# Performance work log

Hardware: AMD Instinct MI355X
Metric: run time of the kernel (lower is better)

## Reference

```python
import jax, jax.numpy as jnp
import numpy as np

NUM_EMBEDDINGS = 1024
EMBEDDING_DIM = 256


def setup_inputs() -> dict:
    key = jax.random.key(0)
    kx, kc = jax.random.split(key)
    x = jax.random.normal(kx, (32, 256, 64, 64), dtype=jnp.float32)
    # codebook initialized uniform(-1/K, 1/K) as in the torch module
    codebook = jax.random.uniform(
        kc, (NUM_EMBEDDINGS, EMBEDDING_DIM), dtype=jnp.float32,
        minval=-1.0 / NUM_EMBEDDINGS, maxval=1.0 / NUM_EMBEDDINGS)
    return {"x": x, "codebook": codebook}


def reference(x, codebook):
    # x: (B, C, H, W) -> (B, H, W, C) -> (N, C)
    B, C, H, W = x.shape
    xf = jnp.transpose(x, (0, 2, 3, 1)).reshape(-1, C)  # (N, C)
    dist = (jnp.sum(xf * xf, axis=1, keepdims=True)
            + jnp.sum(codebook * codebook, axis=1)
            - 2.0 * jnp.matmul(xf, codebook.T))
    indices = jnp.argmin(dist, axis=1)[:, None]  # (N, 1), matches torch unsqueeze(1)
    quantized = codebook[indices[:, 0]].reshape(B, H, W, C)  # gather
    quantized = jnp.transpose(quantized, (0, 3, 1, 2))  # (B, C, H, W)
    return indices, quantized
```

## Files before the change

kernel.cpp:

```cpp
#include <hip/hip_runtime.h>
#include <stdint.h>

#define CDIM   256
#define KCODES 1024
#define HWSZ   4096
#define NROWS  131072
#define DELTA_P 4.7e-4f

#define WS_BQ    0
#define WS_IDX   4096
#define WS_CBBF  528384
#define WS_CNT   1052672
#define WS_LIST  1052800
#define WS_SLOT  1577216

typedef __attribute__((ext_vector_type(8))) short short8;
typedef __attribute__((ext_vector_type(4))) float f32x4;

__device__ inline unsigned short bf16rne(float f) {
    uint32_t u = __float_as_uint(f);
    u += 0x7FFF + ((u >> 16) & 1);
    return (unsigned short)(u >> 16);
}

__device__ __forceinline__ unsigned umin32(unsigned a, unsigned b) { return a < b ? a : b; }
__device__ __forceinline__ unsigned umax32(unsigned a, unsigned b) { return a > b ? a : b; }

__device__ __forceinline__ unsigned long long packkey(float s, int k) {
    unsigned b = __float_as_uint(s);
    unsigned m = (b & 0x80000000u) ? ~b : (b | 0x80000000u);
    return ((unsigned long long)m << 32) | (unsigned)k;
}

__global__ void codesq_kernel(const float* __restrict__ cb, float* __restrict__ Bq) {
#pragma clang fp contract(off)
    int k = blockIdx.x * 256 + threadIdx.x;
    if (k >= KCODES) return;
    const float* er = cb + (size_t)k * CDIM;
    float half_s[2];
    for (int h = 0; h < 2; ++h) {
        float r[8];
        #pragma unroll
        for (int j = 0; j < 8; ++j) { float v = er[h*128 + j]; r[j] = v * v; }
        for (int i = 8; i < 128; i += 8) {
            #pragma unroll
            for (int j = 0; j < 8; ++j) { float v = er[h*128 + i + j]; float sq = v*v; r[j] = r[j] + sq; }
        }
        half_s[h] = ((r[0]+r[1]) + (r[2]+r[3])) + ((r[4]+r[5]) + (r[6]+r[7]));
    }
    Bq[k] = half_s[0] + half_s[1];
}

__global__ void cbcvt_kernel(const float* __restrict__ cb, unsigned short* __restrict__ cbbf,
                             int* __restrict__ counter) {
    int i = blockIdx.x * 256 + threadIdx.x;
    float4 v = ((const float4*)cb)[i];
    ushort4 o;
    o.x = bf16rne(v.x); o.y = bf16rne(v.y); o.z = bf16rne(v.z); o.w = bf16rne(v.w);
    ((ushort4*)cbbf)[i] = o;
    if (i == 0) *counter = 0;
}

__global__ __launch_bounds__(256, 2)
void screen_kernel(const float* __restrict__ x, const unsigned short* __restrict__ cbbf,
                   const float* __restrict__ Bq,
                   int* __restrict__ idx_out, float* __restrict__ outF,
                   int* __restrict__ flag_list, int* __restrict__ counter,
                   unsigned long long* __restrict__ slots) {
    __shared__ unsigned short xs[64 * 264];
    __shared__ unsigned int sRed[4][64][2];

    const int t = threadIdx.x;
    const int w = t >> 6, l = t & 63;
    const int l15 = l & 15, quad = l >> 4;
    const int r0 = blockIdx.x * 64;
    const float* xbase = x + (size_t)(r0 >> 12) * (CDIM * HWSZ) + (r0 & 4095);

    {
        int cbase = (t >> 4) * 2;
        int row4  = (t & 15) * 4;
        for (int it = 0; it < 8; ++it) {
            int c = cbase + it * 32;
            float4 fa = *(const float4*)(xbase + (size_t)c * HWSZ + row4);
            float4 fb = *(const float4*)(xbase + (size_t)(c + 1) * HWSZ + row4);
            *(uint32_t*)&xs[(row4+0)*264 + c] = (uint32_t)bf16rne(fa.x) | ((uint32_t)bf16rne(fb.x) << 16);
            *(uint32_t*)&xs[(row4+1)*264 + c] = (uint32_t)bf16rne(fa.y) | ((uint32_t)bf16rne(fb.y) << 16);
            *(uint32_t*)&xs[(row4+2)*264 + c] = (uint32_t)bf16rne(fa.z) | ((uint32_t)bf16rne(fb.z) << 16);
            *(uint32_t*)&xs[(row4+3)*264 + c] = (uint32_t)bf16rne(fa.w) | ((uint32_t)bf16rne(fb.w) << 16);
        }
    }

    __syncthreads();

    short8 af[8][4];
    #pragma unroll
    for (int step = 0; step < 8; ++step)
        #pragma unroll
        for (int rf = 0; rf < 4; ++rf)
            af[step][rf] = *(const short8*)&xs[(rf*16 + l15)*264 + step*32 + quad*8];

    const unsigned short* bbase = cbbf + (size_t)(w*32 + l15) * CDIM + quad * 8;
    const int kbase = w*32 + l15;

    unsigned int K1[16], K2[16];
    #pragma unroll
    for (int i = 0; i < 16; ++i) { K1[i] = 0xFFFFFFFFu; K2[i] = 0xFFFFFFFFu; }

    for (int kt = 0; kt < 8; ++kt) {
        float bqp0 = Bq[kt*128 + kbase]      + 0.75f;
        float bqp1 = Bq[kt*128 + kbase + 16] + 0.75f;

        f32x4 acc[4][2];
        #pragma unroll
        for (int rf = 0; rf < 4; ++rf)
            #pragma unroll
            for (int cf = 0; cf < 2; ++cf) acc[rf][cf] = (f32x4){0.f, 0.f, 0.f, 0.f};

        #pragma unroll
        for (int step = 0; step < 8; ++step) {
            int koff = step * 32;
            short8 bfr0 = *(const short8*)(bbase + (size_t)(kt*128)      * CDIM + koff);
            short8 bfr1 = *(const short8*)(bbase + (size_t)(kt*128 + 16) * CDIM + koff);
            #pragma unroll
            for (int rf = 0; rf < 4; ++rf) {
                acc[rf][0] = __builtin_amdgcn_mfma_f32_16x16x32_bf16(af[step][rf], bfr0, acc[rf][0], 0, 0, 0);
                acc[rf][1] = __builtin_amdgcn_mfma_f32_16x16x32_bf16(af[step][rf], bfr1, acc[rf][1], 0, 0, 0);
            }
        }

        unsigned int kk0 = (unsigned)(kt*128 + kbase);
        unsigned int kk1 = kk0 + 16u;
        #pragma unroll
        for (int rf = 0; rf < 4; ++rf)
            #pragma unroll
            for (int reg = 0; reg < 4; ++reg) {
                int st = rf*4 + reg;
                {
                    float s = fmaf(-2.f, acc[rf][0][reg], bqp0);
                    unsigned int key = (__float_as_uint(s) & 0xFFFFFC00u) | kk0;
                    unsigned int t1 = umin32(key, K1[st]);
                    unsigned int t2 = umax32(key, K1[st]);
                    K1[st] = t1;
                    K2[st] = umin32(t2, K2[st]);
                }
                {
                    float s = fmaf(-2.f, acc[rf][1][reg], bqp1);
                    unsigned int key = (__float_as_uint(s) & 0xFFFFFC00u) | kk1;
                    unsigned int t1 = umin32(key, K1[st]);
                    unsigned int t2 = umax32(key, K1[st]);
                    K1[st] = t1;
                    K2[st] = umin32(t2, K2[st]);
                }
            }
    }

    #pragma unroll
    for (int st = 0; st < 16; ++st) {
        #pragma unroll
        for (int m = 1; m < 16; m <<= 1) {
            unsigned int o1 = (unsigned int)__shfl_xor((int)K1[st], m, 64);
            unsigned int o2 = (unsigned int)__shfl_xor((int)K2[st], m, 64);
            unsigned int n2 = umin32(umax32(K1[st], o1), umin32(K2[st], o2));
            K1[st] = umin32(K1[st], o1);
            K2[st] = n2;
        }
    }
    if (l15 == 0) {
        #pragma unroll
        for (int rf = 0; rf < 4; ++rf)
            #pragma unroll
            for (int reg = 0; reg < 4; ++reg) {
                int r = rf*16 + quad*4 + reg;
                int st = rf*4 + reg;
                sRed[w][r][0] = K1[st];
                sRed[w][r][1] = K2[st];
            }
    }
    __syncthreads();
    if (t < 64) {
        unsigned int A1 = sRed[0][t][0], A2 = sRed[0][t][1];
        #pragma unroll
        for (int ww = 1; ww < 4; ++ww) {
            unsigned int B1 = sRed[ww][t][0], B2 = sRed[ww][t][1];
            unsigned int n2 = umin32(umax32(A1, B1), umin32(A2, B2));
            A1 = umin32(A1, B1);
            A2 = n2;
        }
        int row = r0 + t;
        int k1i = (int)(A1 & 1023u);
        idx_out[row] = k1i;
        outF[row] = (float)k1i;
        float v1 = __uint_as_float(A1 & 0xFFFFFC00u);
        float v2 = __uint_as_float(A2 & 0xFFFFFC00u);
        if (!(v2 - v1 > DELTA_P)) {
            int pos = atomicAdd(counter, 1);
            flag_list[pos] = row;
            slots[pos] = 0xFFFFFFFFFFFFFFFFull;
        }
    }
}

__global__ __launch_bounds__(256)
void rescore_kernel(const float* __restrict__ x, const float* __restrict__ cb,
                    const float* __restrict__ Bq,
                    const int* __restrict__ flag_list, const int* __restrict__ counter,
                    unsigned long long* __restrict__ slots) {
    __shared__ float xsh[64 * 256];
    __shared__ float cbs[64 * 256];
    __shared__ float sA[64];
    __shared__ int   rows_s[64];

    int cnt = *counter;
    int nbat = (cnt + 63) >> 6;
    int nwork = nbat * 4;
    for (int wk = blockIdx.x; wk < nwork; wk += gridDim.x) {
        int bat = wk >> 2;
        int wq  = wk & 3;
        __syncthreads();
        if (threadIdx.x < 64) {
            int j = bat * 64 + threadIdx.x;
            rows_s[threadIdx.x] = (j < cnt) ? flag_list[j] : -1;
        }
        __syncthreads();
        {
            int rr = threadIdx.x >> 2;
            int c0 = (threadIdx.x & 3) * 64;
            int row = rows_s[rr]; if (row < 0) row = rows_s[0];
            const float* xr = x + (size_t)(row >> 12) * (CDIM * HWSZ) + (row & 4095);
            #pragma unroll 8
            for (int j = 0; j < 64; ++j)
                xsh[rr*256 + c0 + j] = xr[(size_t)(c0 + j) * HWSZ];
        }
        __syncthreads();
        if (threadIdx.x < 64) {
#pragma clang fp contract(off)
            const float* xr = &xsh[threadIdx.x * 256];
            float hs[2];
            for (int h = 0; h < 2; ++h) {
                float rr8[8];
                #pragma unroll
                for (int j = 0; j < 8; ++j) { float v = xr[h*128 + j]; rr8[j] = v * v; }
                for (int i = 8; i < 128; i += 8) {
                    #pragma unroll
                    for (int j = 0; j < 8; ++j) { float v = xr[h*128 + i + j]; float sq = v*v; rr8[j] = rr8[j] + sq; }
                }
                hs[h] = ((rr8[0]+rr8[1]) + (rr8[2]+rr8[3])) + ((rr8[4]+rr8[5]) + (rr8[6]+rr8[7]));
            }
            sA[threadIdx.x] = hs[0] + hs[1];
        }
        __syncthreads();

        const int rq = threadIdx.x >> 4;
        const int cq = threadIdx.x & 15;
        const int sw = cq & 7;
        float Ar[4];
        #pragma unroll
        for (int i = 0; i < 4; ++i) Ar[i] = sA[rq*4 + i];

        float bv[4]; int bk[4];
        #pragma unroll
        for (int i = 0; i < 4; ++i) { bv[i] = 3.4e38f; bk[i] = 0; }

        for (int tile = 0; tile < 4; ++tile) {
            int kt0 = wq * 256 + tile * 64;
            __syncthreads();
            {
                int kc = threadIdx.x >> 2, seg = threadIdx.x & 3;
                const float* crow = cb + (size_t)(kt0 + kc) * CDIM + seg * 64;
                float* dst = &cbs[kc * 256];
                int kw = kc & 7;
                #pragma unroll
                for (int i = 0; i < 16; ++i) {
                    int lc = seg*16 + i;
                    *(float4*)&dst[(lc ^ kw) * 4] = *(const float4*)&crow[i*4];
                }
            }
            __syncthreads();
            float bq[4];
            #pragma unroll
            for (int j = 0; j < 4; ++j) bq[j] = Bq[kt0 + cq + j*16];

            const float* eb[4];
            #pragma unroll
            for (int j = 0; j < 4; ++j) eb[j] = &cbs[(cq + j*16) * 256];
            const float* xb[4];
            #pragma unroll
            for (int i = 0; i < 4; ++i) xb[i] = &xsh[(rq*4 + i) * 256];

            float acc[4][4];
            #pragma unroll
            for (int i = 0; i < 4; ++i)
                #pragma unroll
                for (int j = 0; j < 4; ++j) acc[i][j] = 0.f;

            #pragma unroll 2
            for (int c4 = 0; c4 < 64; ++c4) {
                int so = (c4 ^ sw) * 4;
                float4 ev[4], xv[4];
                #pragma unroll
                for (int j = 0; j < 4; ++j) ev[j] = *(const float4*)&eb[j][so];
                #pragma unroll
                for (int i = 0; i < 4; ++i) xv[i] = *(const float4*)&xb[i][c4*4];
                #pragma unroll
                for (int i = 0; i < 4; ++i)
                    #pragma unroll
                    for (int j = 0; j < 4; ++j) {
                        float a = acc[i][j];
                        a = fmaf(xv[i].x, ev[j].x, a);
                        a = fmaf(xv[i].y, ev[j].y, a);
                        a = fmaf(xv[i].z, ev[j].z, a);
                        a = fmaf(xv[i].w, ev[j].w, a);
                        acc[i][j] = a;
                    }
            }
            #pragma unroll
            for (int j = 0; j < 4; ++j) {
                int k = kt0 + cq + j*16;
                #pragma unroll
                for (int i = 0; i < 4; ++i) {
                    float T1 = Ar[i] + bq[j];
                    float s  = T1 - 2.0f * acc[i][j];
                    if (s < bv[i]) { bv[i] = s; bk[i] = k; }
                }
            }
        }
        #pragma unroll
        for (int i = 0; i < 4; ++i) {
            float b = bv[i]; int k = bk[i];
            #pragma unroll
            for (int m = 1; m < 16; m <<= 1) {
                float ov = __shfl_xor(b, m, 64);
                int   ok = __shfl_xor(k, m, 64);
                if (ov < b || (ov == b && ok < k)) { b = ov; k = ok; }
            }
            bv[i] = b; bk[i] = k;
        }
        if (cq == 0) {
            #pragma unroll
            for (int i = 0; i < 4; ++i) {
                int j = bat * 64 + rq*4 + i;
                if (j < cnt) atomicMin(&slots[j], packkey(bv[i], bk[i]));
            }
        }
    }
}

__global__ void fixup_kernel(const unsigned long long* __restrict__ slots,
                             const int* __restrict__ flag_list,
                             const int* __restrict__ counter,
                             int* __restrict__ idx_out, float* __restrict__ outF) {
    int cnt = *counter;
    int t = blockIdx.x * 256 + threadIdx.x;
    if (t >= cnt) return;
    int row = flag_list[t];
    int k = (int)(unsigned)(slots[t] & 0xFFFFFFFFull);
    idx_out[row] = k;
    outF[row] = (float)k;
}

__global__ __launch_bounds__(256)
void gather_kernel(const float* __restrict__ cb, const int* __restrict__ idx,
                   float* __restrict__ out) {
    __shared__ int   sIdx[64];
    __shared__ float tile[64 * 129];
    const int t  = threadIdx.x;
    const int bh = blockIdx.x;
    const int b  = bh >> 6, h = bh & 63;

    if (t < 64) {
        int id = idx[bh * 64 + t];
        sIdx[t] = id;
        out[bh * 64 + t] = (float)id;
    }
    __syncthreads();

    float* qout = out + NROWS + (size_t)b * (CDIM * HWSZ) + h * 64;

    for (int c0 = 0; c0 < CDIM; c0 += 128) {
        if (c0) __syncthreads();
        {
            int ww = t >> 2, seg = t & 3;
            const float* crow = cb + (size_t)sIdx[ww] * CDIM + c0;
            #pragma unroll
            for (int jj = 0; jj < 8; ++jj) {
                int f = seg + 4 * jj;
                float4 v = *(const float4*)(crow + 4 * f);
                float* dst = &tile[ww * 129 + 4 * f];
                dst[0] = v.x; dst[1] = v.y; dst[2] = v.z; dst[3] = v.w;
            }
        }
        __syncthreads();
        {
            int g = t >> 4, w4 = (t & 15) * 4;
            #pragma unroll
            for (int it = 0; it < 8; ++it) {
                int cl = it * 16 + g;
                float4 v;
                v.x = tile[(w4 + 0) * 129 + cl];
                v.y = tile[(w4 + 1) * 129 + cl];
                v.z = tile[(w4 + 2) * 129 + cl];
                v.w = tile[(w4 + 3) * 129 + cl];
                *(float4*)(qout + (size_t)(c0 + cl) * HWSZ + w4) = v;
            }
        }
    }
}

extern "C" void kernel_launch(void* const* d_in, const int* in_sizes, int n_in,
                              void* d_out, int out_size, void* d_ws, size_t ws_size,
                              hipStream_t stream) {
    const float* x  = (const float*)d_in[0];
    const float* cb = (const float*)d_in[1];
    char* ws = (char*)d_ws;
    float*              Bq    = (float*)(ws + WS_BQ);
    int*                idxbf = (int*)(ws + WS_IDX);
    unsigned short*     cbbf  = (unsigned short*)(ws + WS_CBBF);
    int*                cnt   = (int*)(ws + WS_CNT);
    int*                list  = (int*)(ws + WS_LIST);
    unsigned long long* slots = (unsigned long long*)(ws + WS_SLOT);
    float*              out   = (float*)d_out;

    codesq_kernel<<<KCODES / 256, 256, 0, stream>>>(cb, Bq);
    cbcvt_kernel <<<256, 256, 0, stream>>>(cb, cbbf, cnt);
    screen_kernel<<<NROWS / 64, 256, 0, stream>>>(x, cbbf, Bq, idxbf, out, list, cnt, slots);
    rescore_kernel<<<2048, 256, 0, stream>>>(x, cb, Bq, list, cnt, slots);
    fixup_kernel <<<NROWS / 256, 256, 0, stream>>>(slots, list, cnt, idxbf, out);
    gather_kernel<<<32 * 64, 256, 0, stream>>>(cb, idxbf, out);
}
```

Before: 575.1 us.

## Compact flagged rows once and read codebook directly in rescore

```diff
diff --git a/kernel.cpp b/kernel.cpp
--- a/kernel.cpp
+++ b/kernel.cpp
@@ -13,6 +13,7 @@
 #define WS_CNT   1052672
 #define WS_LIST  1052800
 #define WS_SLOT  1577216
+#define WS_XC    2625792
 
 typedef __attribute__((ext_vector_type(8))) short short8;
 typedef __attribute__((ext_vector_type(4))) float f32x4;
@@ -201,21 +202,39 @@
 }
 
 __global__ __launch_bounds__(256)
+void xcopy_kernel(const float* __restrict__ x, const int* __restrict__ flag_list,
+                  const int* __restrict__ counter, float* __restrict__ xc, int capn) {
+    int cnt = *counter; if (cnt > capn) cnt = capn;
+    for (int base = blockIdx.x * 64; base < cnt; base += gridDim.x * 64) {
+        int j = base + (threadIdx.x >> 2);
+        if (j < cnt) {
+            int row = flag_list[j];
+            const float* xr = x + (size_t)(row >> 12) * (CDIM * HWSZ) + (row & 4095);
+            int c0 = (threadIdx.x & 3) * 64;
+            float* dst = xc + (size_t)j * CDIM + c0;
+            #pragma unroll 8
+            for (int c = 0; c < 64; ++c)
+                dst[c] = xr[(size_t)(c0 + c) * HWSZ];
+        }
+    }
+}
+
+__global__ __launch_bounds__(256, 2)
 void rescore_kernel(const float* __restrict__ x, const float* __restrict__ cb,
                     const float* __restrict__ Bq,
                     const int* __restrict__ flag_list, const int* __restrict__ counter,
+                    const float* __restrict__ xc, int capn,
                     unsigned long long* __restrict__ slots) {
     __shared__ float xsh[64 * 256];
-    __shared__ float cbs[64 * 256];
     __shared__ float sA[64];
     __shared__ int   rows_s[64];
 
     int cnt = *counter;
     int nbat = (cnt + 63) >> 6;
-    int nwork = nbat * 4;
+    int nwork = nbat * 8;
     for (int wk = blockIdx.x; wk < nwork; wk += gridDim.x) {
-        int bat = wk >> 2;
-        int wq  = wk & 3;
+        int bat = wk >> 3;
+        int kq  = wk & 7;
         __syncthreads();
         if (threadIdx.x < 64) {
             int j = bat * 64 + threadIdx.x;
@@ -223,26 +242,56 @@
         }
         __syncthreads();
         {
-            int rr = threadIdx.x >> 2;
-            int c0 = (threadIdx.x & 3) * 64;
-            int row = rows_s[rr]; if (row < 0) row = rows_s[0];
-            const float* xr = x + (size_t)(row >> 12) * (CDIM * HWSZ) + (row & 4095);
-            #pragma unroll 8
-            for (int j = 0; j < 64; ++j)
-                xsh[rr*256 + c0 + j] = xr[(size_t)(c0 + j) * HWSZ];
+            int rr  = threadIdx.x >> 2;
+            int seg = threadIdx.x & 3;
+            int c0  = seg * 64;
+            int j   = bat * 64 + rr;
+            int row = rows_s[rr];
+            int kw  = rr & 7;
+            float* dstrow = &xsh[rr * 256];
+            if (row >= 0 && j < capn) {
+                const float* src = xc + (size_t)j * CDIM + c0;
+                #pragma unroll
+                for (int i = 0; i < 16; ++i) {
+                    int lc = (c0 >> 2) + i;
+                    *(float4*)&dstrow[(lc ^ kw) << 2] = *(const float4*)&src[i << 2];
+                }
+            } else {
+                int rowx = (row < 0) ? rows_s[0] : row;
+                const float* xr = x + (size_t)(rowx >> 12) * (CDIM * HWSZ) + (rowx & 4095);
+                #pragma unroll 4
+                for (int i = 0; i < 16; ++i) {
+                    int lc = (c0 >> 2) + i;
+                    float4 v;
+                    v.x = xr[(size_t)(c0 + (i<<2) + 0) * HWSZ];
+                    v.y = xr[(size_t)(c0 + (i<<2) + 1) * HWSZ];
+                    v.z = xr[(size_t)(c0 + (i<<2) + 2) * HWSZ];
+                    v.w = xr[(size_t)(c0 + (i<<2) + 3) * HWSZ];
+                    *(float4*)&dstrow[(lc ^ kw) << 2] = v;
+                }
+            }
         }
         __syncthreads();
         if (threadIdx.x < 64) {
 #pragma clang fp contract(off)
             const float* xr = &xsh[threadIdx.x * 256];
+            int kw = threadIdx.x & 7;
             float hs[2];
             for (int h = 0; h < 2; ++h) {
                 float rr8[8];
                 #pragma unroll
-                for (int j = 0; j < 8; ++j) { float v = xr[h*128 + j]; rr8[j] = v * v; }
+                for (int j = 0; j < 8; ++j) {
+                    int c = h*128 + j;
+                    float v = xr[((((c >> 2) ^ kw) << 2) | (c & 3))];
+                    rr8[j] = v * v;
+                }
                 for (int i = 8; i < 128; i += 8) {
                     #pragma unroll
-                    for (int j = 0; j < 8; ++j) { float v = xr[h*128 + i + j]; float sq = v*v; rr8[j] = rr8[j] + sq; }
+                    for (int j = 0; j < 8; ++j) {
+                        int c = h*128 + i + j;
+                        float v = xr[((((c >> 2) ^ kw) << 2) | (c & 3))];
+                        float sq = v*v; rr8[j] = rr8[j] + sq;
+                    }
                 }
                 hs[h] = ((rr8[0]+rr8[1]) + (rr8[2]+rr8[3])) + ((rr8[4]+rr8[5]) + (rr8[6]+rr8[7]));
             }
@@ -252,40 +301,29 @@
 
         const int rq = threadIdx.x >> 4;
         const int cq = threadIdx.x & 15;
-        const int sw = cq & 7;
         float Ar[4];
         #pragma unroll
         for (int i = 0; i < 4; ++i) Ar[i] = sA[rq*4 + i];
+        const float* xb[4]; int xkw[4];
+        #pragma unroll
+        for (int i = 0; i < 4; ++i) {
+            int r = rq*4 + i;
+            xb[i] = &xsh[r * 256];
+            xkw[i] = r & 7;
+        }
 
         float bv[4]; int bk[4];
         #pragma unroll
         for (int i = 0; i < 4; ++i) { bv[i] = 3.4e38f; bk[i] = 0; }
 
-        for (int tile = 0; tile < 4; ++tile) {
-            int kt0 = wq * 256 + tile * 64;
-            __syncthreads();
-            {
-                int kc = threadIdx.x >> 2, seg = threadIdx.x & 3;
-                const float* crow = cb + (size_t)(kt0 + kc) * CDIM + seg * 64;
-                float* dst = &cbs[kc * 256];
-                int kw = kc & 7;
-                #pragma unroll
-                for (int i = 0; i < 16; ++i) {
-                    int lc = seg*16 + i;
-                    *(float4*)&dst[(lc ^ kw) * 4] = *(const float4*)&crow[i*4];
-                }
-            }
-            __syncthreads();
+        for (int tile = 0; tile < 2; ++tile) {
+            int kt0 = kq * 128 + tile * 64;
             float bq[4];
             #pragma unroll
             for (int j = 0; j < 4; ++j) bq[j] = Bq[kt0 + cq + j*16];
-
             const float* eb[4];
             #pragma unroll
-            for (int j = 0; j < 4; ++j) eb[j] = &cbs[(cq + j*16) * 256];
-            const float* xb[4];
-            #pragma unroll
-            for (int i = 0; i < 4; ++i) xb[i] = &xsh[(rq*4 + i) * 256];
+            for (int j = 0; j < 4; ++j) eb[j] = cb + (size_t)(kt0 + cq + j*16) * CDIM;
 
             float acc[4][4];
             #pragma unroll
@@ -295,12 +333,11 @@
 
             #pragma unroll 2
             for (int c4 = 0; c4 < 64; ++c4) {
-                int so = (c4 ^ sw) * 4;
                 float4 ev[4], xv[4];
                 #pragma unroll
-                for (int j = 0; j < 4; ++j) ev[j] = *(const float4*)&eb[j][so];
-                #pragma unroll
-                for (int i = 0; i < 4; ++i) xv[i] = *(const float4*)&xb[i][c4*4];
+                for (int j = 0; j < 4; ++j) ev[j] = *(const float4*)&eb[j][c4 << 2];
+                #pragma unroll
+                for (int i = 0; i < 4; ++i) xv[i] = *(const float4*)&xb[i][(c4 ^ xkw[i]) << 2];
                 #pragma unroll
                 for (int i = 0; i < 4; ++i)
                     #pragma unroll
@@ -418,12 +455,21 @@
     int*                cnt   = (int*)(ws + WS_CNT);
     int*                list  = (int*)(ws + WS_LIST);
     unsigned long long* slots = (unsigned long long*)(ws + WS_SLOT);
+    float*              xc    = (float*)(ws + WS_XC);
     float*              out   = (float*)d_out;
+
+    int capn = 0;
+    if (ws_size > (size_t)WS_XC) {
+        size_t avail = (ws_size - (size_t)WS_XC) / (CDIM * sizeof(float));
+        capn = (avail > (size_t)NROWS) ? NROWS : (int)avail;
+    }
 
     codesq_kernel<<<KCODES / 256, 256, 0, stream>>>(cb, Bq);
     cbcvt_kernel <<<256, 256, 0, stream>>>(cb, cbbf, cnt);
     screen_kernel<<<NROWS / 64, 256, 0, stream>>>(x, cbbf, Bq, idxbf, out, list, cnt, slots);
-    rescore_kernel<<<2048, 256, 0, stream>>>(x, cb, Bq, list, cnt, slots);
+    if (capn > 0)
+        xcopy_kernel<<<2048, 256, 0, stream>>>(x, list, cnt, xc, capn);
+    rescore_kernel<<<2048, 256, 0, stream>>>(x, cb, Bq, list, cnt, xc, capn, slots);
     fixup_kernel <<<NROWS / 256, 256, 0, stream>>>(slots, list, cnt, idxbf, out);
     gather_kernel<<<32 * 64, 256, 0, stream>>>(cb, idxbf, out);
 }
```

Result: slower. 745.5 us (+29.6%).

## Precompact flagged rows and norms into workspace for finer-grained rescore

Applied to the files above, without the earlier changes.

```diff
diff --git a/kernel.cpp b/kernel.cpp
--- a/kernel.cpp
+++ b/kernel.cpp
@@ -13,6 +13,8 @@
 #define WS_CNT   1052672
 #define WS_LIST  1052800
 #define WS_SLOT  1577216
+#define WS_AS    2625792
+#define WS_XC    3150080
 
 typedef __attribute__((ext_vector_type(8))) short short8;
 typedef __attribute__((ext_vector_type(4))) float f32x4;
@@ -201,106 +203,117 @@
 }
 
 __global__ __launch_bounds__(256)
+void xcopy_kernel(const float* __restrict__ x, const int* __restrict__ flag_list,
+                  const int* __restrict__ counter, float* __restrict__ xc, int capn) {
+    int cnt = *counter; if (cnt > capn) cnt = capn;
+    for (int base = blockIdx.x * 64; base < cnt; base += gridDim.x * 64) {
+        int j = base + (threadIdx.x >> 2);
+        if (j < cnt) {
+            int row = flag_list[j];
+            const float* xr = x + (size_t)(row >> 12) * (CDIM * HWSZ) + (row & 4095);
+            int c0 = (threadIdx.x & 3) * 64;
+            float* dst = xc + (size_t)j * CDIM + c0;
+            #pragma unroll 8
+            for (int c = 0; c < 64; ++c)
+                dst[c] = xr[(size_t)(c0 + c) * HWSZ];
+        }
+    }
+}
+
+__global__ void asq_kernel(const float* __restrict__ x, const float* __restrict__ xc,
+                           const int* __restrict__ flag_list, const int* __restrict__ counter,
+                           float* __restrict__ As, int capn) {
+#pragma clang fp contract(off)
+    int cnt = *counter;
+    int jf = blockIdx.x * 256 + threadIdx.x;
+    if (jf >= cnt) return;
+    const float* src;
+    size_t stride;
+    if (jf < capn) { src = xc + (size_t)jf * CDIM; stride = 1; }
+    else {
+        int row = flag_list[jf];
+        src = x + (size_t)(row >> 12) * (CDIM * HWSZ) + (row & 4095);
+        stride = HWSZ;
+    }
+    float half_s[2];
+    for (int h = 0; h < 2; ++h) {
+        float r[8];
+        #pragma unroll
+        for (int j = 0; j < 8; ++j) { float v = src[(size_t)(h*128 + j) * stride]; r[j] = v * v; }
+        for (int i = 8; i < 128; i += 8) {
+            #pragma unroll
+            for (int j = 0; j < 8; ++j) { float v = src[(size_t)(h*128 + i + j) * stride]; float sq = v*v; r[j] = r[j] + sq; }
+        }
+        half_s[h] = ((r[0]+r[1]) + (r[2]+r[3])) + ((r[4]+r[5]) + (r[6]+r[7]));
+    }
+    As[jf] = half_s[0] + half_s[1];
+}
+
+__global__ __launch_bounds__(256, 2)
 void rescore_kernel(const float* __restrict__ x, const float* __restrict__ cb,
                     const float* __restrict__ Bq,
                     const int* __restrict__ flag_list, const int* __restrict__ counter,
+                    const float* __restrict__ xc, const float* __restrict__ As, int capn,
                     unsigned long long* __restrict__ slots) {
-    __shared__ float xsh[64 * 256];
     __shared__ float cbs[64 * 256];
-    __shared__ float sA[64];
-    __shared__ int   rows_s[64];
 
     int cnt = *counter;
-    int nbat = (cnt + 63) >> 6;
-    int nwork = nbat * 4;
+    if (cnt <= 0) return;
+    int nbat  = (cnt + 63) >> 6;
+    int nwork = nbat << 4;
     for (int wk = blockIdx.x; wk < nwork; wk += gridDim.x) {
-        int bat = wk >> 2;
-        int wq  = wk & 3;
-        __syncthreads();
-        if (threadIdx.x < 64) {
-            int j = bat * 64 + threadIdx.x;
-            rows_s[threadIdx.x] = (j < cnt) ? flag_list[j] : -1;
-        }
+        int bat = wk >> 4;
+        int kt0 = (wk & 15) << 6;
         __syncthreads();
         {
-            int rr = threadIdx.x >> 2;
-            int c0 = (threadIdx.x & 3) * 64;
-            int row = rows_s[rr]; if (row < 0) row = rows_s[0];
-            const float* xr = x + (size_t)(row >> 12) * (CDIM * HWSZ) + (row & 4095);
-            #pragma unroll 8
-            for (int j = 0; j < 64; ++j)
-                xsh[rr*256 + c0 + j] = xr[(size_t)(c0 + j) * HWSZ];
-        }
-        __syncthreads();
-        if (threadIdx.x < 64) {
-#pragma clang fp contract(off)
-            const float* xr = &xsh[threadIdx.x * 256];
-            float hs[2];
-            for (int h = 0; h < 2; ++h) {
-                float rr8[8];
-                #pragma unroll
-                for (int j = 0; j < 8; ++j) { float v = xr[h*128 + j]; rr8[j] = v * v; }
-                for (int i = 8; i < 128; i += 8) {
-                    #pragma unroll
-                    for (int j = 0; j < 8; ++j) { float v = xr[h*128 + i + j]; float sq = v*v; rr8[j] = rr8[j] + sq; }
-                }
-                hs[h] = ((rr8[0]+rr8[1]) + (rr8[2]+rr8[3])) + ((rr8[4]+rr8[5]) + (rr8[6]+rr8[7]));
-            }
-            sA[threadIdx.x] = hs[0] + hs[1];
+            int kc = threadIdx.x >> 2, seg = threadIdx.x & 3;
+            const float* crow = cb + (size_t)(kt0 + kc) * CDIM + seg * 64;
+            float* dst = &cbs[kc * 256];
+            int kw = kc & 7;
+            #pragma unroll
+            for (int i2 = 0; i2 < 16; ++i2) {
+                int lc = seg*16 + i2;
+                *(float4*)&dst[(lc ^ kw) << 2] = *(const float4*)&crow[i2 << 2];
+            }
         }
         __syncthreads();
 
         const int rq = threadIdx.x >> 4;
         const int cq = threadIdx.x & 15;
         const int sw = cq & 7;
-        float Ar[4];
-        #pragma unroll
-        for (int i = 0; i < 4; ++i) Ar[i] = sA[rq*4 + i];
-
-        float bv[4]; int bk[4];
-        #pragma unroll
-        for (int i = 0; i < 4; ++i) { bv[i] = 3.4e38f; bk[i] = 0; }
-
-        for (int tile = 0; tile < 4; ++tile) {
-            int kt0 = wq * 256 + tile * 64;
-            __syncthreads();
-            {
-                int kc = threadIdx.x >> 2, seg = threadIdx.x & 3;
-                const float* crow = cb + (size_t)(kt0 + kc) * CDIM + seg * 64;
-                float* dst = &cbs[kc * 256];
-                int kw = kc & 7;
-                #pragma unroll
-                for (int i = 0; i < 16; ++i) {
-                    int lc = seg*16 + i;
-                    *(float4*)&dst[(lc ^ kw) * 4] = *(const float4*)&crow[i*4];
-                }
-            }
-            __syncthreads();
-            float bq[4];
-            #pragma unroll
-            for (int j = 0; j < 4; ++j) bq[j] = Bq[kt0 + cq + j*16];
-
-            const float* eb[4];
-            #pragma unroll
-            for (int j = 0; j < 4; ++j) eb[j] = &cbs[(cq + j*16) * 256];
+        const int j0 = bat * 64 + rq * 4;
+
+        int jc[4]; float Ar[4];
+        #pragma unroll
+        for (int i = 0; i < 4; ++i) {
+            int jj = j0 + i;
+            jc[i] = (jj < cnt) ? jj : (cnt - 1);
+            Ar[i] = As[jc[i]];
+        }
+        float bq[4]; const float* eb[4];
+        #pragma unroll
+        for (int j = 0; j < 4; ++j) {
+            bq[j] = Bq[kt0 + cq + j*16];
+            eb[j] = &cbs[(cq + j*16) * 256];
+        }
+
+        float acc[4][4];
+        #pragma unroll
+        for (int i = 0; i < 4; ++i)
+            #pragma unroll
+            for (int j = 0; j < 4; ++j) acc[i][j] = 0.f;
+
+        if (jc[3] < capn) {
             const float* xb[4];
             #pragma unroll
-            for (int i = 0; i < 4; ++i) xb[i] = &xsh[(rq*4 + i) * 256];
-
-            float acc[4][4];
-            #pragma unroll
-            for (int i = 0; i < 4; ++i)
-                #pragma unroll
-                for (int j = 0; j < 4; ++j) acc[i][j] = 0.f;
-
+            for (int i = 0; i < 4; ++i) xb[i] = xc + (size_t)jc[i] * CDIM;
             #pragma unroll 2
             for (int c4 = 0; c4 < 64; ++c4) {
-                int so = (c4 ^ sw) * 4;
                 float4 ev[4], xv[4];
                 #pragma unroll
-                for (int j = 0; j < 4; ++j) ev[j] = *(const float4*)&eb[j][so];
-                #pragma unroll
-                for (int i = 0; i < 4; ++i) xv[i] = *(const float4*)&xb[i][c4*4];
+                for (int j = 0; j < 4; ++j) ev[j] = *(const float4*)&eb[j][(c4 ^ sw) << 2];
+                #pragma unroll
+                for (int i = 0; i < 4; ++i) xv[i] = *(const float4*)&xb[i][c4 << 2];
                 #pragma unroll
                 for (int i = 0; i < 4; ++i)
                     #pragma unroll
@@ -313,15 +326,49 @@
                         acc[i][j] = a;
                     }
             }
-            #pragma unroll
-            for (int j = 0; j < 4; ++j) {
-                int k = kt0 + cq + j*16;
+        } else {
+            const float* xb[4];
+            #pragma unroll
+            for (int i = 0; i < 4; ++i) {
+                int row = flag_list[jc[i]];
+                xb[i] = x + (size_t)(row >> 12) * (CDIM * HWSZ) + (row & 4095);
+            }
+            for (int c4 = 0; c4 < 64; ++c4) {
+                float4 ev[4], xv[4];
+                #pragma unroll
+                for (int j = 0; j < 4; ++j) ev[j] = *(const float4*)&eb[j][(c4 ^ sw) << 2];
                 #pragma unroll
                 for (int i = 0; i < 4; ++i) {
-                    float T1 = Ar[i] + bq[j];
-                    float s  = T1 - 2.0f * acc[i][j];
-                    if (s < bv[i]) { bv[i] = s; bk[i] = k; }
+                    xv[i].x = xb[i][(size_t)(c4*4 + 0) * HWSZ];
+                    xv[i].y = xb[i][(size_t)(c4*4 + 1) * HWSZ];
+                    xv[i].z = xb[i][(size_t)(c4*4 + 2) * HWSZ];
+                    xv[i].w = xb[i][(size_t)(c4*4 + 3) * HWSZ];
                 }
+                #pragma unroll
+                for (int i = 0; i < 4; ++i)
+                    #pragma unroll
+                    for (int j = 0; j < 4; ++j) {
+                        float a = acc[i][j];
+                        a = fmaf(xv[i].x, ev[j].x, a);
+                        a = fmaf(xv[i].y, ev[j].y, a);
+                        a = fmaf(xv[i].z, ev[j].z, a);
+                        a = fmaf(xv[i].w, ev[j].w, a);
+                        acc[i][j] = a;
+                    }
+            }
+        }
+
+        float bv[4]; int bk[4];
+        #pragma unroll
+        for (int i = 0; i < 4; ++i) { bv[i] = 3.4e38f; bk[i] = 0; }
+        #pragma unroll
+        for (int j = 0; j < 4; ++j) {
+            int k = kt0 + cq + j*16;
+            #pragma unroll
+            for (int i = 0; i < 4; ++i) {
+                float T1 = Ar[i] + bq[j];
+                float s  = T1 - 2.0f * acc[i][j];
+                if (s < bv[i]) { bv[i] = s; bk[i] = k; }
             }
         }
         #pragma unroll
@@ -338,8 +385,8 @@
         if (cq == 0) {
             #pragma unroll
             for (int i = 0; i < 4; ++i) {
-                int j = bat * 64 + rq*4 + i;
-                if (j < cnt) atomicMin(&slots[j], packkey(bv[i], bk[i]));
+                int jj = j0 + i;
+                if (jj < cnt) atomicMin(&slots[jj], packkey(bv[i], bk[i]));
             }
         }
     }
@@ -418,12 +465,23 @@
     int*                cnt   = (int*)(ws + WS_CNT);
     int*                list  = (int*)(ws + WS_LIST);
     unsigned long long* slots = (unsigned long long*)(ws + WS_SLOT);
+    float*              As    = (float*)(ws + WS_AS);
+    float*              xc    = (float*)(ws + WS_XC);
     float*              out   = (float*)d_out;
+
+    int capn = 0;
+    if (ws_size > (size_t)WS_XC) {
+        size_t avail = (ws_size - (size_t)WS_XC) / (CDIM * sizeof(float));
+        capn = (avail > (size_t)NROWS) ? NROWS : (int)avail;
+    }
 
     codesq_kernel<<<KCODES / 256, 256, 0, stream>>>(cb, Bq);
     cbcvt_kernel <<<256, 256, 0, stream>>>(cb, cbbf, cnt);
     screen_kernel<<<NROWS / 64, 256, 0, stream>>>(x, cbbf, Bq, idxbf, out, list, cnt, slots);
-    rescore_kernel<<<2048, 256, 0, stream>>>(x, cb, Bq, list, cnt, slots);
+    if (capn > 0)
+        xcopy_kernel<<<2048, 256, 0, stream>>>(x, list, cnt, xc, capn);
+    asq_kernel   <<<NROWS / 256, 256, 0, stream>>>(x, xc, list, cnt, As, capn);
+    rescore_kernel<<<2048, 256, 0, stream>>>(x, cb, Bq, list, cnt, xc, As, capn, slots);
     fixup_kernel <<<NROWS / 256, 256, 0, stream>>>(slots, list, cnt, idxbf, out);
     gather_kernel<<<32 * 64, 256, 0, stream>>>(cb, idxbf, out);
 }
```

New measurement: 541.6 us. 5.8% less time.
